# Kernel tuning notes

Hardware: AMD Instinct MI355X
Metric: run time of the kernel (lower is better)

The kernel has to match this reference:

```python
import jax, jax.numpy as jnp
import numpy as np

H = 128  # hidden size


def setup_inputs() -> dict:
    key = jax.random.key(0)
    ks = jax.random.split(key, 7)
    s = 1.0 / np.sqrt(H)
    return {
        "inputs": jax.random.normal(ks[0], (512, 1, 1024, 64), dtype=jnp.float32),
        "W_ih": jax.random.uniform(ks[1], (3 * H, 64), jnp.float32, -s, s),
        "W_hh": jax.random.uniform(ks[2], (3 * H, H), jnp.float32, -s, s),
        "b_ih": jax.random.uniform(ks[3], (3 * H,), jnp.float32, -s, s),
        "b_hh": jax.random.uniform(ks[4], (3 * H,), jnp.float32, -s, s),
        "W_fc": jax.random.uniform(ks[5], (51, H), jnp.float32, -s, s),
        "b_fc": jax.random.uniform(ks[6], (51,), jnp.float32, -s, s),
    }


def _gru_last_hidden(x, W_ih, W_hh, b_ih, b_hh):
    # x: [B, T, I]. Precompute all input-side gate projections in one GEMM.
    B = x.shape[0]
    xg = jnp.einsum("bti,gi->btg", x, W_ih) + b_ih  # [B, T, 3H]
    xg = jnp.swapaxes(xg, 0, 1)  # [T, B, 3H] for scan

    def step(h, xg_t):
        gh = h @ W_hh.T + b_hh  # [B, 3H]
        xr, xz, xn = jnp.split(xg_t, 3, axis=-1)
        hr, hz, hn = jnp.split(gh, 3, axis=-1)
        r = jax.nn.sigmoid(xr + hr)
        z = jax.nn.sigmoid(xz + hz)
        n = jnp.tanh(xn + r * hn)
        h_new = (1.0 - z) * n + z * h
        return h_new, None

    h0 = jnp.zeros((B, H), dtype=x.dtype)
    hT, _ = jax.lax.scan(step, h0, xg)
    return hT  # [B, H]


def reference(inputs, W_ih, W_hh, b_ih, b_hh, W_fc, b_fc):
    x = jnp.squeeze(inputs, axis=1)  # [B, T, 64]
    hT = _gru_last_hidden(x, W_ih, W_hh, b_ih, b_hh)
    return hT @ W_fc.T + b_fc  # [B, 51]
```

## Files before the change

kernel.cpp:

```cpp
#include <hip/hip_runtime.h>
#include <hip/hip_bf16.h>

#define TT    1024
#define BATCH 512
#define HH    128
#define II    64
#define BC    16
#define NTHR  512
#define CHUNK 8
#define XROW  72
#define HROW  136
#define L2E   1.4426950408889634f

typedef __attribute__((ext_vector_type(8))) short bhalf8;
typedef __attribute__((ext_vector_type(4))) short bhalf4;
typedef __attribute__((ext_vector_type(4))) float f32x4;

static __device__ __forceinline__ unsigned cvtpk(float lo, float hi) {
  unsigned r;
  asm("v_cvt_pk_bf16_f32 %0, %1, %2" : "=v"(r) : "v"(lo), "v"(hi));
  return r;
}
static __device__ __forceinline__ float bf2f(short s) {
  return __builtin_bit_cast(float, ((unsigned)(unsigned short)s) << 16);
}
static __device__ __forceinline__ f32x4 mfma16(bhalf8 a, bhalf8 b, f32x4 c) {
  return __builtin_amdgcn_mfma_f32_16x16x32_bf16(a, b, c, 0, 0, 0);
}
static __device__ __forceinline__ bhalf8 packrow8s(const float* p, float s) {
  union { bhalf8 v; unsigned u[4]; } cv;
  cv.u[0] = cvtpk(p[0] * s, p[1] * s);
  cv.u[1] = cvtpk(p[2] * s, p[3] * s);
  cv.u[2] = cvtpk(p[4] * s, p[5] * s);
  cv.u[3] = cvtpk(p[6] * s, p[7] * s);
  return cv.v;
}
static __device__ __forceinline__ void bar_lgkm() {
  asm volatile("s_waitcnt lgkmcnt(0)\n\ts_barrier" ::: "memory");
}

#define DOSTEP(TP, AR, AZ, AHN, AXN, BR, BZ, BHN, BXN)                          \
  {                                                                             \
    constexpr int tp = (TP);                                                    \
    const short* hrow = (tp & 1) ? hrd1 : hrd0;                                 \
    bhalf8 hf0 = *(const bhalf8*)(hrow + q * 8);                                \
    bhalf8 hf1 = *(const bhalf8*)(hrow + 32 + q * 8);                           \
    bhalf8 hf2 = *(const bhalf8*)(hrow + 64 + q * 8);                           \
    bhalf8 hf3 = *(const bhalf8*)(hrow + 96 + q * 8);                           \
    if (tp == 0 && more) {   \
      const float* sA = xsrcA + (size_t)(c + 1) * (CHUNK * II);                 \
      xl0 = *(const float4*)(sA);                                               \
      xl1 = *(const float4*)(sA + 4);                                           \
      xl2 = *(const float4*)(sA + 4 * II);                                      \
      xl3 = *(const float4*)(sA + 4 * II + 4);                                  \
    }                                                                           \
    AR  = mfma16(whh[0][0], hf0, AR);  AR  = mfma16(whh[0][1], hf1, AR);        \
    AR  = mfma16(whh[0][2], hf2, AR);  AR  = mfma16(whh[0][3], hf3, AR);        \
    AZ  = mfma16(whh[1][0], hf0, AZ);  AZ  = mfma16(whh[1][1], hf1, AZ);        \
    AZ  = mfma16(whh[1][2], hf2, AZ);  AZ  = mfma16(whh[1][3], hf3, AZ);        \
    AHN = mfma16(whh[2][0], hf0, AHN); AHN = mfma16(whh[2][1], hf1, AHN);       \
    AHN = mfma16(whh[2][2], hf2, AHN); AHN = mfma16(whh[2][3], hf3, AHN);       \
             \
    {                                                                           \
      const int nb2 = (tp == 7) ? ((c + 1) & 1) : (c & 1);                      \
      const short* xrow = xbase + nb2 * (CHUNK * BC * XROW)                     \
                                + ((tp + 1) & 7) * (BC * XROW);                 \
      bhalf8 xf0 = *(const bhalf8*)(xrow + q * 8);                              \
      bhalf8 xf1 = *(const bhalf8*)(xrow + 32 + q * 8);                         \
      BR  = bias_r;                                                             \
      BR  = mfma16(wih[0][0], xf0, BR);  BR  = mfma16(wih[0][1], xf1, BR);      \
      BZ  = bias_z;                                                             \
      BZ  = mfma16(wih[1][0], xf0, BZ);  BZ  = mfma16(wih[1][1], xf1, BZ);      \
      BXN = bias_xn;                                                            \
      BXN = mfma16(wih[2][0], xf0, BXN); BXN = mfma16(wih[2][1], xf1, BXN);     \
      BHN = bias_hn;                                                            \
    }                                                                           \
                  \
    _Pragma("unroll")                                                           \
    for (int r = 0; r < 4; ++r) {                                               \
      const float rg = __builtin_amdgcn_rcpf(                                   \
          1.0f + __builtin_amdgcn_exp2f(-AR[r]));                               \
      const float zg = __builtin_amdgcn_rcpf(                                   \
          1.0f + __builtin_amdgcn_exp2f(-AZ[r]));                               \
      const float na = fmaf(rg, AHN[r], AXN[r]);                                \
      const float ng = fmaf(-2.0f, __builtin_amdgcn_rcpf(                       \
          __builtin_amdgcn_exp2f(na) + 1.0f), 1.0f);                            \
      hprev[r] = fmaf(zg, hprev[r] - ng, ng);                                   \
    }                                                                           \
    {                                                                           \
      union { bhalf4 v; unsigned u[2]; } hp;                                    \
      hp.u[0] = cvtpk(hprev[0], hprev[1]);                                      \
      hp.u[1] = cvtpk(hprev[2], hprev[3]);                                      \
      *(bhalf4*)((tp & 1) ? hw1 : hw0) = hp.v;                                  \
    }                                                                           \
    if (tp == 4 && more) {          \
      short* xd = xstA + ((c + 1) & 1) * (CHUNK * BC * XROW);                   \
      union { bhalf8 v; unsigned u[4]; } cv;                                    \
      cv.u[0] = cvtpk(xl0.x, xl0.y); cv.u[1] = cvtpk(xl0.z, xl0.w);             \
      cv.u[2] = cvtpk(xl1.x, xl1.y); cv.u[3] = cvtpk(xl1.z, xl1.w);             \
      *(bhalf8*)xd = cv.v;                                                      \
      cv.u[0] = cvtpk(xl2.x, xl2.y); cv.u[1] = cvtpk(xl2.z, xl2.w);             \
      cv.u[2] = cvtpk(xl3.x, xl3.y); cv.u[3] = cvtpk(xl3.z, xl3.w);             \
      *(bhalf8*)(xd + 4 * (BC * XROW)) = cv.v;                                  \
    }                                                                           \
    bar_lgkm();                                                                 \
  }

__global__ __launch_bounds__(NTHR) __attribute__((amdgpu_waves_per_eu(2, 2)))
void gru_fused(
    const float* __restrict__ xin, const float* __restrict__ Wih,
    const float* __restrict__ Whh, const float* __restrict__ bih,
    const float* __restrict__ bhh, const float* __restrict__ Wfc,
    const float* __restrict__ bfc, float* __restrict__ out)
{
  __shared__ short xsh[2][CHUNK][BC * XROW];
  __shared__ short hsh[2][BC * HROW];

  const int tid = threadIdx.x;
  const int lane = tid & 63;
  const int wv = tid >> 6;
  const int q = lane >> 4;
  const int c15 = lane & 15;
  const int b0 = blockIdx.x * BC;

  bhalf8 whh[3][4];
  bhalf8 wih[3][2];
#pragma unroll
  for (int g = 0; g < 3; ++g) {
    const float sc = (g == 2) ? 2.0f * L2E : L2E;
    const int grow = g * HH + wv * 16 + c15;
#pragma unroll
    for (int kt = 0; kt < 4; ++kt)
      whh[g][kt] = packrow8s(Whh + grow * HH + kt * 32 + q * 8, sc);
#pragma unroll
    for (int kt = 0; kt < 2; ++kt)
      wih[g][kt] = packrow8s(Wih + grow * II + kt * 32 + q * 8, sc);
  }

  f32x4 bias_r, bias_z, bias_hn, bias_xn;
#pragma unroll
  for (int r = 0; r < 4; ++r) {
    const int d = wv * 16 + q * 4 + r;
    bias_r[r]  = (bih[d] + bhh[d]) * L2E;
    bias_z[r]  = (bih[HH + d] + bhh[HH + d]) * L2E;
    bias_xn[r] = bih[2 * HH + d] * (2.0f * L2E);
    bias_hn[r] = bhh[2 * HH + d] * (2.0f * L2E);
  }

  for (int i = tid; i < BC * HROW; i += NTHR) hsh[0][i] = 0;

  const int tpA = tid >> 7, bs = (tid >> 3) & 15, g8 = tid & 7;
  const float* xsrcA = xin + (size_t)(b0 + bs) * (TT * II) + tpA * II + g8 * 8;
  short* xstA = &xsh[0][tpA][bs * XROW + g8 * 8];

  float4 xl0, xl1, xl2, xl3;
  {
    float4 a0 = *(const float4*)(xsrcA);
    float4 a1 = *(const float4*)(xsrcA + 4);
    float4 a2 = *(const float4*)(xsrcA + 4 * II);
    float4 a3 = *(const float4*)(xsrcA + 4 * II + 4);
    union { bhalf8 v; unsigned u[4]; } cv;
    cv.u[0] = cvtpk(a0.x, a0.y); cv.u[1] = cvtpk(a0.z, a0.w);
    cv.u[2] = cvtpk(a1.x, a1.y); cv.u[3] = cvtpk(a1.z, a1.w);
    *(bhalf8*)xstA = cv.v;
    cv.u[0] = cvtpk(a2.x, a2.y); cv.u[1] = cvtpk(a2.z, a2.w);
    cv.u[2] = cvtpk(a3.x, a3.y); cv.u[3] = cvtpk(a3.z, a3.w);
    *(bhalf8*)(xstA + 4 * (BC * XROW)) = cv.v;
  }
  __syncthreads();

  const short* hrd0 = &hsh[0][c15 * HROW];
  const short* hrd1 = &hsh[1][c15 * HROW];
  short* hw0 = &hsh[1][c15 * HROW + wv * 16 + q * 4];
  short* hw1 = &hsh[0][c15 * HROW + wv * 16 + q * 4];
  const short* xbase = &xsh[0][0][c15 * XROW];

  f32x4 hprev = {0.f, 0.f, 0.f, 0.f};
  f32x4 aR, aZ, aHN, aXN, bR, bZ, bHN, bXN;

  {
    const short* xrow = xbase;
    bhalf8 xf0 = *(const bhalf8*)(xrow + q * 8);
    bhalf8 xf1 = *(const bhalf8*)(xrow + 32 + q * 8);
    aR  = bias_r;
    aR  = mfma16(wih[0][0], xf0, aR);  aR  = mfma16(wih[0][1], xf1, aR);
    aZ  = bias_z;
    aZ  = mfma16(wih[1][0], xf0, aZ);  aZ  = mfma16(wih[1][1], xf1, aZ);
    aXN = bias_xn;
    aXN = mfma16(wih[2][0], xf0, aXN); aXN = mfma16(wih[2][1], xf1, aXN);
    aHN = bias_hn;
  }

#pragma unroll 1
  for (int c = 0; c < TT / CHUNK; ++c) {
    const int more = (c + 1 < TT / CHUNK);
    DOSTEP(0, aR, aZ, aHN, aXN, bR, bZ, bHN, bXN)
    DOSTEP(1, bR, bZ, bHN, bXN, aR, aZ, aHN, aXN)
    DOSTEP(2, aR, aZ, aHN, aXN, bR, bZ, bHN, bXN)
    DOSTEP(3, bR, bZ, bHN, bXN, aR, aZ, aHN, aXN)
    DOSTEP(4, aR, aZ, aHN, aXN, bR, bZ, bHN, bXN)
    DOSTEP(5, bR, bZ, bHN, bXN, aR, aZ, aHN, aXN)
    DOSTEP(6, aR, aZ, aHN, aXN, bR, bZ, bHN, bXN)
    DOSTEP(7, bR, bZ, bHN, bXN, aR, aZ, aHN, aXN)
  }

  for (int idx = tid; idx < BC * 51; idx += NTHR) {
    const int bb = idx / 51;
    const int o = idx - bb * 51;
    const float* wf = Wfc + o * HH;
    const short* hr = &hsh[0][bb * HROW];
    float s = bfc[o];
#pragma unroll
    for (int d = 0; d < HH; d += 4) {
      const float4 wvv = *(const float4*)(wf + d);
      s += bf2f(hr[d]) * wvv.x + bf2f(hr[d + 1]) * wvv.y
         + bf2f(hr[d + 2]) * wvv.z + bf2f(hr[d + 3]) * wvv.w;
    }
    out[(size_t)(b0 + bb) * 51 + o] = s;
  }
}

extern "C" void kernel_launch(void* const* d_in, const int* in_sizes, int n_in,
                              void* d_out, int out_size, void* d_ws, size_t ws_size,
                              hipStream_t stream) {
  const float* xin = (const float*)d_in[0];
  const float* Wih = (const float*)d_in[1];
  const float* Whh = (const float*)d_in[2];
  const float* bih = (const float*)d_in[3];
  const float* bhh = (const float*)d_in[4];
  const float* Wfc = (const float*)d_in[5];
  const float* bfc = (const float*)d_in[6];
  float* o = (float*)d_out;
  hipLaunchKernelGGL(gru_fused, dim3(BATCH / BC), dim3(NTHR), 0, stream,
                     xin, Wih, Whh, bih, bhh, Wfc, bfc, o);
}
```

Measured before the change: 608.7 us.

## Halve block to four waves, each computing two hidden-row tiles per step

Cuts threads per block from 512 to 256, so each wave owns 32 hidden units (two 16-row MFMA tiles) instead of 16, with doubled register-resident weights and biases and each thread loading four x slices per chunk. The per-step work is also reordered: sigmoid evaluation is interleaved with the input-side MFMAs for the next step, and the hn bias is folded into the MFMA accumulator init. The aim is fewer waves meeting at each per-timestep barrier and more independent MFMA work per wave to hide latency. In exchange, register pressure rises and occupancy is pinned to one wave per EU.

```diff
diff --git a/kernel.cpp b/kernel.cpp
--- a/kernel.cpp
+++ b/kernel.cpp
@@ -6,7 +6,7 @@
 #define HH    128
 #define II    64
 #define BC    16
-#define NTHR  512
+#define NTHR  256
 #define CHUNK 8
 #define XROW  72
 #define HROW  136
@@ -39,74 +39,116 @@
   asm volatile("s_waitcnt lgkmcnt(0)\n\ts_barrier" ::: "memory");
 }
 
-#define DOSTEP(TP, AR, AZ, AHN, AXN, BR, BZ, BHN, BXN)                          \
-  {                                                                             \
-    constexpr int tp = (TP);                                                    \
-    const short* hrow = (tp & 1) ? hrd1 : hrd0;                                 \
-    bhalf8 hf0 = *(const bhalf8*)(hrow + q * 8);                                \
-    bhalf8 hf1 = *(const bhalf8*)(hrow + 32 + q * 8);                           \
-    bhalf8 hf2 = *(const bhalf8*)(hrow + 64 + q * 8);                           \
-    bhalf8 hf3 = *(const bhalf8*)(hrow + 96 + q * 8);                           \
-    if (tp == 0 && more) {   \
-      const float* sA = xsrcA + (size_t)(c + 1) * (CHUNK * II);                 \
-      xl0 = *(const float4*)(sA);                                               \
-      xl1 = *(const float4*)(sA + 4);                                           \
-      xl2 = *(const float4*)(sA + 4 * II);                                      \
-      xl3 = *(const float4*)(sA + 4 * II + 4);                                  \
-    }                                                                           \
-    AR  = mfma16(whh[0][0], hf0, AR);  AR  = mfma16(whh[0][1], hf1, AR);        \
-    AR  = mfma16(whh[0][2], hf2, AR);  AR  = mfma16(whh[0][3], hf3, AR);        \
-    AZ  = mfma16(whh[1][0], hf0, AZ);  AZ  = mfma16(whh[1][1], hf1, AZ);        \
-    AZ  = mfma16(whh[1][2], hf2, AZ);  AZ  = mfma16(whh[1][3], hf3, AZ);        \
-    AHN = mfma16(whh[2][0], hf0, AHN); AHN = mfma16(whh[2][1], hf1, AHN);       \
-    AHN = mfma16(whh[2][2], hf2, AHN); AHN = mfma16(whh[2][3], hf3, AHN);       \
-             \
-    {                                                                           \
-      const int nb2 = (tp == 7) ? ((c + 1) & 1) : (c & 1);                      \
-      const short* xrow = xbase + nb2 * (CHUNK * BC * XROW)                     \
-                                + ((tp + 1) & 7) * (BC * XROW);                 \
-      bhalf8 xf0 = *(const bhalf8*)(xrow + q * 8);                              \
-      bhalf8 xf1 = *(const bhalf8*)(xrow + 32 + q * 8);                         \
-      BR  = bias_r;                                                             \
-      BR  = mfma16(wih[0][0], xf0, BR);  BR  = mfma16(wih[0][1], xf1, BR);      \
-      BZ  = bias_z;                                                             \
-      BZ  = mfma16(wih[1][0], xf0, BZ);  BZ  = mfma16(wih[1][1], xf1, BZ);      \
-      BXN = bias_xn;                                                            \
-      BXN = mfma16(wih[2][0], xf0, BXN); BXN = mfma16(wih[2][1], xf1, BXN);     \
-      BHN = bias_hn;                                                            \
-    }                                                                           \
-                  \
-    _Pragma("unroll")                                                           \
-    for (int r = 0; r < 4; ++r) {                                               \
-      const float rg = __builtin_amdgcn_rcpf(                                   \
-          1.0f + __builtin_amdgcn_exp2f(-AR[r]));                               \
-      const float zg = __builtin_amdgcn_rcpf(                                   \
-          1.0f + __builtin_amdgcn_exp2f(-AZ[r]));                               \
-      const float na = fmaf(rg, AHN[r], AXN[r]);                                \
-      const float ng = fmaf(-2.0f, __builtin_amdgcn_rcpf(                       \
-          __builtin_amdgcn_exp2f(na) + 1.0f), 1.0f);                            \
-      hprev[r] = fmaf(zg, hprev[r] - ng, ng);                                   \
-    }                                                                           \
-    {                                                                           \
-      union { bhalf4 v; unsigned u[2]; } hp;                                    \
-      hp.u[0] = cvtpk(hprev[0], hprev[1]);                                      \
-      hp.u[1] = cvtpk(hprev[2], hprev[3]);                                      \
-      *(bhalf4*)((tp & 1) ? hw1 : hw0) = hp.v;                                  \
-    }                                                                           \
-    if (tp == 4 && more) {          \
-      short* xd = xstA + ((c + 1) & 1) * (CHUNK * BC * XROW);                   \
-      union { bhalf8 v; unsigned u[4]; } cv;                                    \
-      cv.u[0] = cvtpk(xl0.x, xl0.y); cv.u[1] = cvtpk(xl0.z, xl0.w);             \
-      cv.u[2] = cvtpk(xl1.x, xl1.y); cv.u[3] = cvtpk(xl1.z, xl1.w);             \
-      *(bhalf8*)xd = cv.v;                                                      \
-      cv.u[0] = cvtpk(xl2.x, xl2.y); cv.u[1] = cvtpk(xl2.z, xl2.w);             \
-      cv.u[2] = cvtpk(xl3.x, xl3.y); cv.u[3] = cvtpk(xl3.z, xl3.w);             \
-      *(bhalf8*)(xd + 4 * (BC * XROW)) = cv.v;                                  \
-    }                                                                           \
-    bar_lgkm();                                                                 \
-  }
-
-__global__ __launch_bounds__(NTHR) __attribute__((amdgpu_waves_per_eu(2, 2)))
+#define SIG1(x) __builtin_amdgcn_rcpf(1.0f + __builtin_amdgcn_exp2f(-(x)))
+
+#define NUPD(RG0, RG1, RG2, RG3, ZG0, ZG1, ZG2, ZG3, AHN, AXN, HP, WEXPR)      \
+  {                                                                            \
+    const float na0 = fmaf(RG0, AHN[0], AXN[0]);                               \
+    const float na1 = fmaf(RG1, AHN[1], AXN[1]);                               \
+    const float na2 = fmaf(RG2, AHN[2], AXN[2]);                               \
+    const float na3 = fmaf(RG3, AHN[3], AXN[3]);                               \
+    const float ng0 = fmaf(-2.0f,                                              \
+        __builtin_amdgcn_rcpf(__builtin_amdgcn_exp2f(na0) + 1.0f), 1.0f);      \
+    const float ng1 = fmaf(-2.0f,                                              \
+        __builtin_amdgcn_rcpf(__builtin_amdgcn_exp2f(na1) + 1.0f), 1.0f);      \
+    const float ng2 = fmaf(-2.0f,                                              \
+        __builtin_amdgcn_rcpf(__builtin_amdgcn_exp2f(na2) + 1.0f), 1.0f);      \
+    const float ng3 = fmaf(-2.0f,                                              \
+        __builtin_amdgcn_rcpf(__builtin_amdgcn_exp2f(na3) + 1.0f), 1.0f);      \
+    HP[0] = fmaf(ZG0, HP[0] - ng0, ng0);                                       \
+    HP[1] = fmaf(ZG1, HP[1] - ng1, ng1);                                       \
+    HP[2] = fmaf(ZG2, HP[2] - ng2, ng2);                                       \
+    HP[3] = fmaf(ZG3, HP[3] - ng3, ng3);                                       \
+    union { bhalf4 v; unsigned u[2]; } hp_;                                    \
+    hp_.u[0] = cvtpk(HP[0], HP[1]);                                            \
+    hp_.u[1] = cvtpk(HP[2], HP[3]);                                            \
+    *(bhalf4*)(WEXPR) = hp_.v;                                                 \
+  }
+
+#define XMFMA(G, BA0, BA1, BI0, BI1, XF0, XF1)                                 \
+  BA0 = mfma16(wih[G][0][0], XF0, BI0);                                        \
+  BA0 = mfma16(wih[G][0][1], XF1, BA0);                                        \
+  BA1 = mfma16(wih[G][1][0], XF0, BI1);                                        \
+  BA1 = mfma16(wih[G][1][1], XF1, BA1);
+
+#define DOSTEP(TP, AR0, AR1, AZ0, AZ1, AXN0, AXN1,                             \
+               BR0, BR1, BZ0, BZ1, BXN0, BXN1)                                 \
+  {                                                                            \
+    constexpr int tp = (TP);                                                   \
+    const short* hrow = (tp & 1) ? hrd1 : hrd0;                                \
+    bhalf8 hf0 = *(const bhalf8*)(hrow + q * 8);                               \
+    bhalf8 hf1 = *(const bhalf8*)(hrow + 32 + q * 8);                          \
+    bhalf8 hf2 = *(const bhalf8*)(hrow + 64 + q * 8);                          \
+    bhalf8 hf3 = *(const bhalf8*)(hrow + 96 + q * 8);                          \
+    const int nb2 = (tp == 7) ? ((c + 1) & 1) : (c & 1);                       \
+    const short* xrow = xbase + nb2 * (CHUNK * BC * XROW)                      \
+                              + ((tp + 1) & 7) * (BC * XROW);                  \
+    bhalf8 xf0 = *(const bhalf8*)(xrow + q * 8);                               \
+    bhalf8 xf1 = *(const bhalf8*)(xrow + 32 + q * 8);                          \
+    if (tp == 0 && more) {                  \
+      const size_t off_ = (size_t)(c + 1) * (CHUNK * II);                      \
+      xl0 = *(const float4*)(xsrc0 + off_);                                    \
+      xl1 = *(const float4*)(xsrc0 + off_ + 4);                                \
+      xl2 = *(const float4*)(xsrc1 + off_);                                    \
+      xl3 = *(const float4*)(xsrc1 + off_ + 4);                                \
+      xl4 = *(const float4*)(xsrc2 + off_);                                    \
+      xl5 = *(const float4*)(xsrc2 + off_ + 4);                                \
+      xl6 = *(const float4*)(xsrc3 + off_);                                    \
+      xl7 = *(const float4*)(xsrc3 + off_ + 4);                                \
+    }                                                                          \
+                                    \
+    AR0 = mfma16(whh[0][0][0], hf0, AR0); AR0 = mfma16(whh[0][0][1], hf1, AR0);\
+    AR0 = mfma16(whh[0][0][2], hf2, AR0); AR0 = mfma16(whh[0][0][3], hf3, AR0);\
+    AR1 = mfma16(whh[0][1][0], hf0, AR1); AR1 = mfma16(whh[0][1][1], hf1, AR1);\
+    AR1 = mfma16(whh[0][1][2], hf2, AR1); AR1 = mfma16(whh[0][1][3], hf3, AR1);\
+    AZ0 = mfma16(whh[1][0][0], hf0, AZ0); AZ0 = mfma16(whh[1][0][1], hf1, AZ0);\
+    AZ0 = mfma16(whh[1][0][2], hf2, AZ0); AZ0 = mfma16(whh[1][0][3], hf3, AZ0);\
+    AZ1 = mfma16(whh[1][1][0], hf0, AZ1); AZ1 = mfma16(whh[1][1][1], hf1, AZ1);\
+    AZ1 = mfma16(whh[1][1][2], hf2, AZ1); AZ1 = mfma16(whh[1][1][3], hf3, AZ1);\
+    f32x4 ahn0 = mfma16(whh[2][0][0], hf0, bias_hn0);                          \
+    ahn0 = mfma16(whh[2][0][1], hf1, ahn0);                                    \
+    ahn0 = mfma16(whh[2][0][2], hf2, ahn0);                                    \
+    ahn0 = mfma16(whh[2][0][3], hf3, ahn0);                                    \
+    f32x4 ahn1 = mfma16(whh[2][1][0], hf0, bias_hn1);                          \
+    ahn1 = mfma16(whh[2][1][1], hf1, ahn1);                                    \
+    ahn1 = mfma16(whh[2][1][2], hf2, ahn1);                                    \
+    ahn1 = mfma16(whh[2][1][3], hf3, ahn1);                                    \
+            \
+    const float r0g0 = SIG1(AR0[0]), r0g1 = SIG1(AR0[1]);                      \
+    const float r0g2 = SIG1(AR0[2]), r0g3 = SIG1(AR0[3]);                      \
+    const float r1g0 = SIG1(AR1[0]), r1g1 = SIG1(AR1[1]);                      \
+    const float r1g2 = SIG1(AR1[2]), r1g3 = SIG1(AR1[3]);                      \
+    XMFMA(0, BR0, BR1, bias_r0, bias_r1, xf0, xf1)                             \
+    const float z0g0 = SIG1(AZ0[0]), z0g1 = SIG1(AZ0[1]);                      \
+    const float z0g2 = SIG1(AZ0[2]), z0g3 = SIG1(AZ0[3]);                      \
+    const float z1g0 = SIG1(AZ1[0]), z1g1 = SIG1(AZ1[1]);                      \
+    const float z1g2 = SIG1(AZ1[2]), z1g3 = SIG1(AZ1[3]);                      \
+    XMFMA(1, BZ0, BZ1, bias_z0, bias_z1, xf0, xf1)                             \
+    NUPD(r0g0, r0g1, r0g2, r0g3, z0g0, z0g1, z0g2, z0g3, ahn0, AXN0, hp0,      \
+         ((tp & 1) ? hw1 : hw0))                                               \
+    NUPD(r1g0, r1g1, r1g2, r1g3, z1g0, z1g1, z1g2, z1g3, ahn1, AXN1, hp1,      \
+         ((tp & 1) ? hw1 : hw0) + 16)                                          \
+    XMFMA(2, BXN0, BXN1, bias_xn0, bias_xn1, xf0, xf1)                         \
+    if (tp == 4 && more) {         \
+      const int bo = ((c + 1) & 1) * (CHUNK * BC * XROW);                      \
+      union { bhalf8 v; unsigned u[4]; } cv;                                   \
+      cv.u[0] = cvtpk(xl0.x, xl0.y); cv.u[1] = cvtpk(xl0.z, xl0.w);            \
+      cv.u[2] = cvtpk(xl1.x, xl1.y); cv.u[3] = cvtpk(xl1.z, xl1.w);            \
+      *(bhalf8*)(xst0 + bo) = cv.v;                                            \
+      cv.u[0] = cvtpk(xl2.x, xl2.y); cv.u[1] = cvtpk(xl2.z, xl2.w);            \
+      cv.u[2] = cvtpk(xl3.x, xl3.y); cv.u[3] = cvtpk(xl3.z, xl3.w);            \
+      *(bhalf8*)(xst1 + bo) = cv.v;                                            \
+      cv.u[0] = cvtpk(xl4.x, xl4.y); cv.u[1] = cvtpk(xl4.z, xl4.w);            \
+      cv.u[2] = cvtpk(xl5.x, xl5.y); cv.u[3] = cvtpk(xl5.z, xl5.w);            \
+      *(bhalf8*)(xst2 + bo) = cv.v;                                            \
+      cv.u[0] = cvtpk(xl6.x, xl6.y); cv.u[1] = cvtpk(xl6.z, xl6.w);            \
+      cv.u[2] = cvtpk(xl7.x, xl7.y); cv.u[3] = cvtpk(xl7.z, xl7.w);            \
+      *(bhalf8*)(xst3 + bo) = cv.v;                                            \
+    }                                                                          \
+    bar_lgkm();                                                                \
+  }
+
+__global__ __launch_bounds__(NTHR) __attribute__((amdgpu_waves_per_eu(1, 1)))
 void gru_fused(
     const float* __restrict__ xin, const float* __restrict__ Wih,
     const float* __restrict__ Whh, const float* __restrict__ bih,
@@ -123,85 +165,105 @@
   const int c15 = lane & 15;
   const int b0 = blockIdx.x * BC;
 
-  bhalf8 whh[3][4];
-  bhalf8 wih[3][2];
+  bhalf8 whh[3][2][4];
+  bhalf8 wih[3][2][2];
 #pragma unroll
   for (int g = 0; g < 3; ++g) {
     const float sc = (g == 2) ? 2.0f * L2E : L2E;
-    const int grow = g * HH + wv * 16 + c15;
-#pragma unroll
-    for (int kt = 0; kt < 4; ++kt)
-      whh[g][kt] = packrow8s(Whh + grow * HH + kt * 32 + q * 8, sc);
-#pragma unroll
-    for (int kt = 0; kt < 2; ++kt)
-      wih[g][kt] = packrow8s(Wih + grow * II + kt * 32 + q * 8, sc);
-  }
-
-  f32x4 bias_r, bias_z, bias_hn, bias_xn;
+#pragma unroll
+    for (int mt = 0; mt < 2; ++mt) {
+      const int grow = g * HH + wv * 32 + mt * 16 + c15;
+#pragma unroll
+      for (int kt = 0; kt < 4; ++kt)
+        whh[g][mt][kt] = packrow8s(Whh + grow * HH + kt * 32 + q * 8, sc);
+#pragma unroll
+      for (int kt = 0; kt < 2; ++kt)
+        wih[g][mt][kt] = packrow8s(Wih + grow * II + kt * 32 + q * 8, sc);
+    }
+  }
+
+  f32x4 bias_r0, bias_r1, bias_z0, bias_z1, bias_hn0, bias_hn1, bias_xn0, bias_xn1;
 #pragma unroll
   for (int r = 0; r < 4; ++r) {
-    const int d = wv * 16 + q * 4 + r;
-    bias_r[r]  = (bih[d] + bhh[d]) * L2E;
-    bias_z[r]  = (bih[HH + d] + bhh[HH + d]) * L2E;
-    bias_xn[r] = bih[2 * HH + d] * (2.0f * L2E);
-    bias_hn[r] = bhh[2 * HH + d] * (2.0f * L2E);
+    const int d0 = wv * 32 + q * 4 + r;
+    const int d1 = d0 + 16;
+    bias_r0[r]  = (bih[d0] + bhh[d0]) * L2E;
+    bias_r1[r]  = (bih[d1] + bhh[d1]) * L2E;
+    bias_z0[r]  = (bih[HH + d0] + bhh[HH + d0]) * L2E;
+    bias_z1[r]  = (bih[HH + d1] + bhh[HH + d1]) * L2E;
+    bias_xn0[r] = bih[2 * HH + d0] * (2.0f * L2E);
+    bias_xn1[r] = bih[2 * HH + d1] * (2.0f * L2E);
+    bias_hn0[r] = bhh[2 * HH + d0] * (2.0f * L2E);
+    bias_hn1[r] = bhh[2 * HH + d1] * (2.0f * L2E);
   }
 
   for (int i = tid; i < BC * HROW; i += NTHR) hsh[0][i] = 0;
 
-  const int tpA = tid >> 7, bs = (tid >> 3) & 15, g8 = tid & 7;
-  const float* xsrcA = xin + (size_t)(b0 + bs) * (TT * II) + tpA * II + g8 * 8;
-  short* xstA = &xsh[0][tpA][bs * XROW + g8 * 8];
-
-  float4 xl0, xl1, xl2, xl3;
+  const int tpA0 = tid >> 7,           bsA0 = (tid >> 3) & 15,           g8A = tid & 7;
+  const int tpA1 = (tid + 256) >> 7,   bsA1 = ((tid + 256) >> 3) & 15;
+  const int tpA2 = (tid + 512) >> 7,   bsA2 = ((tid + 512) >> 3) & 15;
+  const int tpA3 = (tid + 768) >> 7,   bsA3 = ((tid + 768) >> 3) & 15;
+  const float* xsrc0 = xin + (size_t)(b0 + bsA0) * (TT * II) + tpA0 * II + g8A * 8;
+  const float* xsrc1 = xin + (size_t)(b0 + bsA1) * (TT * II) + tpA1 * II + g8A * 8;
+  const float* xsrc2 = xin + (size_t)(b0 + bsA2) * (TT * II) + tpA2 * II + g8A * 8;
+  const float* xsrc3 = xin + (size_t)(b0 + bsA3) * (TT * II) + tpA3 * II + g8A * 8;
+  short* xst0 = &xsh[0][tpA0][bsA0 * XROW + g8A * 8];
+  short* xst1 = &xsh[0][tpA1][bsA1 * XROW + g8A * 8];
+  short* xst2 = &xsh[0][tpA2][bsA2 * XROW + g8A * 8];
+  short* xst3 = &xsh[0][tpA3][bsA3 * XROW + g8A * 8];
+
+  float4 xl0, xl1, xl2, xl3, xl4, xl5, xl6, xl7;
   {
-    float4 a0 = *(const float4*)(xsrcA);
-    float4 a1 = *(const float4*)(xsrcA + 4);
-    float4 a2 = *(const float4*)(xsrcA + 4 * II);
-    float4 a3 = *(const float4*)(xsrcA + 4 * II + 4);
     union { bhalf8 v; unsigned u[4]; } cv;
-    cv.u[0] = cvtpk(a0.x, a0.y); cv.u[1] = cvtpk(a0.z, a0.w);
-    cv.u[2] = cvtpk(a1.x, a1.y); cv.u[3] = cvtpk(a1.z, a1.w);
-    *(bhalf8*)xstA = cv.v;
-    cv.u[0] = cvtpk(a2.x, a2.y); cv.u[1] = cvtpk(a2.z, a2.w);
-    cv.u[2] = cvtpk(a3.x, a3.y); cv.u[3] = cvtpk(a3.z, a3.w);
-    *(bhalf8*)(xstA + 4 * (BC * XROW)) = cv.v;
+    float4 a, b;
+    a = *(const float4*)(xsrc0); b = *(const float4*)(xsrc0 + 4);
+    cv.u[0] = cvtpk(a.x, a.y); cv.u[1] = cvtpk(a.z, a.w);
+    cv.u[2] = cvtpk(b.x, b.y); cv.u[3] = cvtpk(b.z, b.w);
+    *(bhalf8*)xst0 = cv.v;
+    a = *(const float4*)(xsrc1); b = *(const float4*)(xsrc1 + 4);
+    cv.u[0] = cvtpk(a.x, a.y); cv.u[1] = cvtpk(a.z, a.w);
+    cv.u[2] = cvtpk(b.x, b.y); cv.u[3] = cvtpk(b.z, b.w);
+    *(bhalf8*)xst1 = cv.v;
+    a = *(const float4*)(xsrc2); b = *(const float4*)(xsrc2 + 4);
+    cv.u[0] = cvtpk(a.x, a.y); cv.u[1] = cvtpk(a.z, a.w);
+    cv.u[2] = cvtpk(b.x, b.y); cv.u[3] = cvtpk(b.z, b.w);
+    *(bhalf8*)xst2 = cv.v;
+    a = *(const float4*)(xsrc3); b = *(const float4*)(xsrc3 + 4);
+    cv.u[0] = cvtpk(a.x, a.y); cv.u[1] = cvtpk(a.z, a.w);
+    cv.u[2] = cvtpk(b.x, b.y); cv.u[3] = cvtpk(b.z, b.w);
+    *(bhalf8*)xst3 = cv.v;
   }
   __syncthreads();
 
   const short* hrd0 = &hsh[0][c15 * HROW];
   const short* hrd1 = &hsh[1][c15 * HROW];
-  short* hw0 = &hsh[1][c15 * HROW + wv * 16 + q * 4];
-  short* hw1 = &hsh[0][c15 * HROW + wv * 16 + q * 4];
+  short* hw0 = &hsh[1][c15 * HROW + wv * 32 + q * 4];
+  short* hw1 = &hsh[0][c15 * HROW + wv * 32 + q * 4];
   const short* xbase = &xsh[0][0][c15 * XROW];
 
-  f32x4 hprev = {0.f, 0.f, 0.f, 0.f};
-  f32x4 aR, aZ, aHN, aXN, bR, bZ, bHN, bXN;
+  f32x4 hp0 = {0.f, 0.f, 0.f, 0.f};
+  f32x4 hp1 = {0.f, 0.f, 0.f, 0.f};
+  f32x4 aR0, aR1, aZ0, aZ1, aXN0, aXN1, bR0, bR1, bZ0, bZ1, bXN0, bXN1;
 
   {
-    const short* xrow = xbase;
-    bhalf8 xf0 = *(const bhalf8*)(xrow + q * 8);
-    bhalf8 xf1 = *(const bhalf8*)(xrow + 32 + q * 8);
-    aR  = bias_r;
-    aR  = mfma16(wih[0][0], xf0, aR);  aR  = mfma16(wih[0][1], xf1, aR);
-    aZ  = bias_z;
-    aZ  = mfma16(wih[1][0], xf0, aZ);  aZ  = mfma16(wih[1][1], xf1, aZ);
-    aXN = bias_xn;
-    aXN = mfma16(wih[2][0], xf0, aXN); aXN = mfma16(wih[2][1], xf1, aXN);
-    aHN = bias_hn;
+    bhalf8 xf0 = *(const bhalf8*)(xbase + q * 8);
+    bhalf8 xf1 = *(const bhalf8*)(xbase + 32 + q * 8);
+    XMFMA(0, aR0, aR1, bias_r0, bias_r1, xf0, xf1)
+    XMFMA(1, aZ0, aZ1, bias_z0, bias_z1, xf0, xf1)
+    XMFMA(2, aXN0, aXN1, bias_xn0, bias_xn1, xf0, xf1)
   }
 
 #pragma unroll 1
   for (int c = 0; c < TT / CHUNK; ++c) {
     const int more = (c + 1 < TT / CHUNK);
-    DOSTEP(0, aR, aZ, aHN, aXN, bR, bZ, bHN, bXN)
-    DOSTEP(1, bR, bZ, bHN, bXN, aR, aZ, aHN, aXN)
-    DOSTEP(2, aR, aZ, aHN, aXN, bR, bZ, bHN, bXN)
-    DOSTEP(3, bR, bZ, bHN, bXN, aR, aZ, aHN, aXN)
-    DOSTEP(4, aR, aZ, aHN, aXN, bR, bZ, bHN, bXN)
-    DOSTEP(5, bR, bZ, bHN, bXN, aR, aZ, aHN, aXN)
-    DOSTEP(6, aR, aZ, aHN, aXN, bR, bZ, bHN, bXN)
-    DOSTEP(7, bR, bZ, bHN, bXN, aR, aZ, aHN, aXN)
+    DOSTEP(0, aR0, aR1, aZ0, aZ1, aXN0, aXN1, bR0, bR1, bZ0, bZ1, bXN0, bXN1)
+    DOSTEP(1, bR0, bR1, bZ0, bZ1, bXN0, bXN1, aR0, aR1, aZ0, aZ1, aXN0, aXN1)
+    DOSTEP(2, aR0, aR1, aZ0, aZ1, aXN0, aXN1, bR0, bR1, bZ0, bZ1, bXN0, bXN1)
+    DOSTEP(3, bR0, bR1, bZ0, bZ1, bXN0, bXN1, aR0, aR1, aZ0, aZ1, aXN0, aXN1)
+    DOSTEP(4, aR0, aR1, aZ0, aZ1, aXN0, aXN1, bR0, bR1, bZ0, bZ1, bXN0, bXN1)
+    DOSTEP(5, bR0, bR1, bZ0, bZ1, bXN0, bXN1, aR0, aR1, aZ0, aZ1, aXN0, aXN1)
+    DOSTEP(6, aR0, aR1, aZ0, aZ1, aXN0, aXN1, bR0, bR1, bZ0, bZ1, bXN0, bXN1)
+    DOSTEP(7, bR0, bR1, bZ0, bZ1, bXN0, bXN1, aR0, aR1, aZ0, aZ1, aXN0, aXN1)
   }
 
   for (int idx = tid; idx < BC * 51; idx += NTHR) {
```

New measurement: 677.0 us. +11.2%, slower.

## Reorder GRU step so gate math precedes barrier and fuse input projection into gate MFMAs

Applied to the files above, without the earlier changes.

Restructures each recurrent step so the gate nonlinearities for the previous accumulators run first, then the barrier, then one fused MFMA chain per gate that adds both the W_hh·h and W_ih·x contributions to the bias. The separate one-step-ahead input projection goes away. A dummy first step (z-gate forced to saturate) primes the pipeline, and a trailing GATES call finishes the last step. The x prefetch is now unconditional, reloading the last chunk on the final iteration. This shortens the instruction sequence between barriers. In exchange, the input MFMAs now sit on the serial h-dependent critical path instead of being overlapped with it.

```diff
diff --git a/kernel.cpp b/kernel.cpp
--- a/kernel.cpp
+++ b/kernel.cpp
@@ -39,61 +39,78 @@
   asm volatile("s_waitcnt lgkmcnt(0)\n\ts_barrier" ::: "memory");
 }
 
+#define SIG1(x) __builtin_amdgcn_rcpf(1.0f + __builtin_amdgcn_exp2f(-(x)))
+
+#define GATES(AR, AZ, AHN, AXN, HWPTR)                                          \
+  {                                                                             \
+    const float rg0 = SIG1(AR[0]), rg1 = SIG1(AR[1]);                           \
+    const float rg2 = SIG1(AR[2]), rg3 = SIG1(AR[3]);                           \
+    const float zg0 = SIG1(AZ[0]), zg1 = SIG1(AZ[1]);                           \
+    const float zg2 = SIG1(AZ[2]), zg3 = SIG1(AZ[3]);                           \
+    const float na0 = fmaf(rg0, AHN[0], AXN[0]);                                \
+    const float na1 = fmaf(rg1, AHN[1], AXN[1]);                                \
+    const float na2 = fmaf(rg2, AHN[2], AXN[2]);                                \
+    const float na3 = fmaf(rg3, AHN[3], AXN[3]);                                \
+    const float ng0 = fmaf(-2.0f,                                               \
+        __builtin_amdgcn_rcpf(__builtin_amdgcn_exp2f(na0) + 1.0f), 1.0f);       \
+    const float ng1 = fmaf(-2.0f,                                               \
+        __builtin_amdgcn_rcpf(__builtin_amdgcn_exp2f(na1) + 1.0f), 1.0f);       \
+    const float ng2 = fmaf(-2.0f,                                               \
+        __builtin_amdgcn_rcpf(__builtin_amdgcn_exp2f(na2) + 1.0f), 1.0f);       \
+    const float ng3 = fmaf(-2.0f,                                               \
+        __builtin_amdgcn_rcpf(__builtin_amdgcn_exp2f(na3) + 1.0f), 1.0f);       \
+    hprev[0] = fmaf(zg0, hprev[0] - ng0, ng0);                                  \
+    hprev[1] = fmaf(zg1, hprev[1] - ng1, ng1);                                  \
+    hprev[2] = fmaf(zg2, hprev[2] - ng2, ng2);                                  \
+    hprev[3] = fmaf(zg3, hprev[3] - ng3, ng3);                                  \
+    union { bhalf4 v; unsigned u[2]; } hp;                                      \
+    hp.u[0] = cvtpk(hprev[0], hprev[1]);                                        \
+    hp.u[1] = cvtpk(hprev[2], hprev[3]);                                        \
+    *(bhalf4*)(HWPTR) = hp.v;                                                   \
+  }
+
 #define DOSTEP(TP, AR, AZ, AHN, AXN, BR, BZ, BHN, BXN)                          \
   {                                                                             \
     constexpr int tp = (TP);                                                    \
+    if constexpr (tp == 0) {  \
+      const float* sA = xsrcA + (size_t)cn * (CHUNK * II);                      \
+      xl0 = *(const float4*)(sA);                                               \
+      xl1 = *(const float4*)(sA + 4);                                           \
+      xl2 = *(const float4*)(sA + 4 * II);                                      \
+      xl3 = *(const float4*)(sA + 4 * II + 4);                                  \
+    }                                                                           \
+    GATES(AR, AZ, AHN, AXN, (tp & 1) ? hwr1 : hwr0)                             \
+    bar_lgkm();                                                                 \
+         \
     const short* hrow = (tp & 1) ? hrd1 : hrd0;                                 \
     bhalf8 hf0 = *(const bhalf8*)(hrow + q * 8);                                \
     bhalf8 hf1 = *(const bhalf8*)(hrow + 32 + q * 8);                           \
     bhalf8 hf2 = *(const bhalf8*)(hrow + 64 + q * 8);                           \
     bhalf8 hf3 = *(const bhalf8*)(hrow + 96 + q * 8);                           \
-    if (tp == 0 && more) {   \
-      const float* sA = xsrcA + (size_t)(c + 1) * (CHUNK * II);                 \
-      xl0 = *(const float4*)(sA);                                               \
-      xl1 = *(const float4*)(sA + 4);                                           \
-      xl2 = *(const float4*)(sA + 4 * II);                                      \
-      xl3 = *(const float4*)(sA + 4 * II + 4);                                  \
-    }                                                                           \
-    AR  = mfma16(whh[0][0], hf0, AR);  AR  = mfma16(whh[0][1], hf1, AR);        \
-    AR  = mfma16(whh[0][2], hf2, AR);  AR  = mfma16(whh[0][3], hf3, AR);        \
-    AZ  = mfma16(whh[1][0], hf0, AZ);  AZ  = mfma16(whh[1][1], hf1, AZ);        \
-    AZ  = mfma16(whh[1][2], hf2, AZ);  AZ  = mfma16(whh[1][3], hf3, AZ);        \
-    AHN = mfma16(whh[2][0], hf0, AHN); AHN = mfma16(whh[2][1], hf1, AHN);       \
-    AHN = mfma16(whh[2][2], hf2, AHN); AHN = mfma16(whh[2][3], hf3, AHN);       \
-             \
-    {                                                                           \
-      const int nb2 = (tp == 7) ? ((c + 1) & 1) : (c & 1);                      \
-      const short* xrow = xbase + nb2 * (CHUNK * BC * XROW)                     \
-                                + ((tp + 1) & 7) * (BC * XROW);                 \
-      bhalf8 xf0 = *(const bhalf8*)(xrow + q * 8);                              \
-      bhalf8 xf1 = *(const bhalf8*)(xrow + 32 + q * 8);                         \
-      BR  = bias_r;                                                             \
-      BR  = mfma16(wih[0][0], xf0, BR);  BR  = mfma16(wih[0][1], xf1, BR);      \
-      BZ  = bias_z;                                                             \
-      BZ  = mfma16(wih[1][0], xf0, BZ);  BZ  = mfma16(wih[1][1], xf1, BZ);      \
-      BXN = bias_xn;                                                            \
-      BXN = mfma16(wih[2][0], xf0, BXN); BXN = mfma16(wih[2][1], xf1, BXN);     \
-      BHN = bias_hn;                                                            \
-    }                                                                           \
-                  \
-    _Pragma("unroll")                                                           \
-    for (int r = 0; r < 4; ++r) {                                               \
-      const float rg = __builtin_amdgcn_rcpf(                                   \
-          1.0f + __builtin_amdgcn_exp2f(-AR[r]));                               \
-      const float zg = __builtin_amdgcn_rcpf(                                   \
-          1.0f + __builtin_amdgcn_exp2f(-AZ[r]));                               \
-      const float na = fmaf(rg, AHN[r], AXN[r]);                                \
-      const float ng = fmaf(-2.0f, __builtin_amdgcn_rcpf(                       \
-          __builtin_amdgcn_exp2f(na) + 1.0f), 1.0f);                            \
-      hprev[r] = fmaf(zg, hprev[r] - ng, ng);                                   \
-    }                                                                           \
-    {                                                                           \
-      union { bhalf4 v; unsigned u[2]; } hp;                                    \
-      hp.u[0] = cvtpk(hprev[0], hprev[1]);                                      \
-      hp.u[1] = cvtpk(hprev[2], hprev[3]);                                      \
-      *(bhalf4*)((tp & 1) ? hw1 : hw0) = hp.v;                                  \
-    }                                                                           \
-    if (tp == 4 && more) {          \
+    const short* xrow = xbase + (c & 1) * (CHUNK * BC * XROW)                   \
+                              + tp * (BC * XROW);                               \
+    bhalf8 xf0 = *(const bhalf8*)(xrow + q * 8);                                \
+    bhalf8 xf1 = *(const bhalf8*)(xrow + 32 + q * 8);                           \
+                            \
+    BR  = mfma16(whh[0][0], hf0, bias_r);                                       \
+    BR  = mfma16(whh[0][1], hf1, BR);                                           \
+    BR  = mfma16(whh[0][2], hf2, BR);                                           \
+    BR  = mfma16(whh[0][3], hf3, BR);                                           \
+    BR  = mfma16(wih[0][0], xf0, BR);                                           \
+    BR  = mfma16(wih[0][1], xf1, BR);                                           \
+    BZ  = mfma16(whh[1][0], hf0, bias_z);                                       \
+    BZ  = mfma16(whh[1][1], hf1, BZ);                                           \
+    BZ  = mfma16(whh[1][2], hf2, BZ);                                           \
+    BZ  = mfma16(whh[1][3], hf3, BZ);                                           \
+    BZ  = mfma16(wih[1][0], xf0, BZ);                                           \
+    BZ  = mfma16(wih[1][1], xf1, BZ);                                           \
+    BHN = mfma16(whh[2][0], hf0, bias_hn);                                      \
+    BHN = mfma16(whh[2][1], hf1, BHN);                                          \
+    BHN = mfma16(whh[2][2], hf2, BHN);                                          \
+    BHN = mfma16(whh[2][3], hf3, BHN);                                          \
+    BXN = mfma16(wih[2][0], xf0, bias_xn);                                      \
+    BXN = mfma16(wih[2][1], xf1, BXN);                                          \
+    if constexpr (tp == 4) {        \
       short* xd = xstA + ((c + 1) & 1) * (CHUNK * BC * XROW);                   \
       union { bhalf8 v; unsigned u[4]; } cv;                                    \
       cv.u[0] = cvtpk(xl0.x, xl0.y); cv.u[1] = cvtpk(xl0.z, xl0.w);             \
@@ -103,7 +120,6 @@
       cv.u[2] = cvtpk(xl3.x, xl3.y); cv.u[3] = cvtpk(xl3.z, xl3.w);             \
       *(bhalf8*)(xd + 4 * (BC * XROW)) = cv.v;                                  \
     }                                                                           \
-    bar_lgkm();                                                                 \
   }
 
 __global__ __launch_bounds__(NTHR) __attribute__((amdgpu_waves_per_eu(2, 2)))
@@ -147,7 +163,7 @@
     bias_hn[r] = bhh[2 * HH + d] * (2.0f * L2E);
   }
 
-  for (int i = tid; i < BC * HROW; i += NTHR) hsh[0][i] = 0;
+  for (int i = tid; i < BC * HROW; i += NTHR) { hsh[0][i] = 0; hsh[1][i] = 0; }
 
   const int tpA = tid >> 7, bs = (tid >> 3) & 15, g8 = tid & 7;
   const float* xsrcA = xin + (size_t)(b0 + bs) * (TT * II) + tpA * II + g8 * 8;
@@ -171,29 +187,20 @@
 
   const short* hrd0 = &hsh[0][c15 * HROW];
   const short* hrd1 = &hsh[1][c15 * HROW];
-  short* hw0 = &hsh[1][c15 * HROW + wv * 16 + q * 4];
-  short* hw1 = &hsh[0][c15 * HROW + wv * 16 + q * 4];
+  short* hwr0 = &hsh[0][c15 * HROW + wv * 16 + q * 4];
+  short* hwr1 = &hsh[1][c15 * HROW + wv * 16 + q * 4];
   const short* xbase = &xsh[0][0][c15 * XROW];
 
   f32x4 hprev = {0.f, 0.f, 0.f, 0.f};
-  f32x4 aR, aZ, aHN, aXN, bR, bZ, bHN, bXN;
-
-  {
-    const short* xrow = xbase;
-    bhalf8 xf0 = *(const bhalf8*)(xrow + q * 8);
-    bhalf8 xf1 = *(const bhalf8*)(xrow + 32 + q * 8);
-    aR  = bias_r;
-    aR  = mfma16(wih[0][0], xf0, aR);  aR  = mfma16(wih[0][1], xf1, aR);
-    aZ  = bias_z;
-    aZ  = mfma16(wih[1][0], xf0, aZ);  aZ  = mfma16(wih[1][1], xf1, aZ);
-    aXN = bias_xn;
-    aXN = mfma16(wih[2][0], xf0, aXN); aXN = mfma16(wih[2][1], xf1, aXN);
-    aHN = bias_hn;
-  }
+  f32x4 aR  = {0.f, 0.f, 0.f, 0.f};
+  f32x4 aZ  = {100.f, 100.f, 100.f, 100.f};
+  f32x4 aHN = {0.f, 0.f, 0.f, 0.f};
+  f32x4 aXN = {0.f, 0.f, 0.f, 0.f};
+  f32x4 bR, bZ, bHN, bXN;
 
 #pragma unroll 1
   for (int c = 0; c < TT / CHUNK; ++c) {
-    const int more = (c + 1 < TT / CHUNK);
+    const int cn = (c + 1 < TT / CHUNK) ? c + 1 : c;
     DOSTEP(0, aR, aZ, aHN, aXN, bR, bZ, bHN, bXN)
     DOSTEP(1, bR, bZ, bHN, bXN, aR, aZ, aHN, aXN)
     DOSTEP(2, aR, aZ, aHN, aXN, bR, bZ, bHN, bXN)
@@ -203,6 +210,9 @@
     DOSTEP(6, aR, aZ, aHN, aXN, bR, bZ, bHN, bXN)
     DOSTEP(7, bR, bZ, bHN, bXN, aR, aZ, aHN, aXN)
   }
+
+  GATES(aR, aZ, aHN, aXN, hwr0)
+  __syncthreads();
 
   for (int idx = tid; idx < BC * 51; idx += NTHR) {
     const int bb = idx / 51;
```

Measured after the change: 628.5 us. 3.3% more time.
